# Kernel optimization log

Hardware: AMD Instinct MI355X
Metric: run time of the kernel (lower is better)

Reference implementation:

```python
import jax, jax.numpy as jnp
import numpy as np

EMB = 1024
HEADS = 16
HEAD_DIM = EMB // HEADS
ROPE_BASE = 10000.0


def rotate_half(x):
    # Interleaved rotate: pairs (x0,x1,x2,x3,...) -> (-x1,x0,-x3,x2,...)
    x1 = x[..., ::2]
    x2 = x[..., 1::2]
    return jnp.stack((-x2, x1), axis=-1).reshape(x.shape)


def rope_cos_sin(seq_len, head_dim):
    inv_freq = 1.0 / (ROPE_BASE ** (jnp.arange(0, head_dim, 2, dtype=jnp.float32) / head_dim))
    pos = jnp.arange(seq_len, dtype=jnp.float32)
    freqs = jnp.outer(pos, inv_freq)            # [S, hd/2]
    emb = jnp.concatenate([freqs, freqs], -1)   # [S, hd]  (NOTE: concat, matching source)
    return jnp.cos(emb)[None, None], jnp.sin(emb)[None, None]  # [1,1,S,hd]


def setup_inputs() -> dict:
    key = jax.random.key(0)
    ks = jax.random.split(key, 5)
    B, S = 2, 2048
    x = jax.random.normal(ks[0], (B, S, EMB), dtype=jnp.float32)
    scale = EMB ** -0.5
    Wq = jax.random.normal(ks[1], (EMB, EMB), dtype=jnp.float32) * scale
    Wk = jax.random.normal(ks[2], (EMB, EMB), dtype=jnp.float32) * scale
    Wv = jax.random.normal(ks[3], (EMB, EMB), dtype=jnp.float32) * scale
    Wo = jax.random.normal(ks[4], (EMB, EMB), dtype=jnp.float32) * scale
    return {"x": x, "Wq": Wq, "Wk": Wk, "Wv": Wv, "Wo": Wo}


def reference(x, Wq, Wk, Wv, Wo):
    B, S, E = x.shape
    def shape_heads(t):
        return t.reshape(B, S, HEADS, HEAD_DIM).transpose(0, 2, 1, 3)  # [B,H,S,hd]
    q = shape_heads(x @ Wq.T)
    k = shape_heads(x @ Wk.T)
    v = shape_heads(x @ Wv.T)
    cos, sin = rope_cos_sin(S, HEAD_DIM)
    q = q * cos + rotate_half(q) * sin
    k = k * cos + rotate_half(k) * sin
    scale = HEAD_DIM ** -0.5
    scores = jnp.einsum('bhqd,bhkd->bhqk', q, k) * scale  # [B,H,S,S]
    causal = jnp.triu(jnp.ones((S, S), dtype=bool), k=1)
    scores = jnp.where(causal, -jnp.inf, scores)
    attn = jax.nn.softmax(scores, axis=-1)
    out = jnp.einsum('bhqk,bhkd->bhqd', attn, v)           # [B,H,S,hd]
    out = out.transpose(0, 2, 1, 3).reshape(B, S, E)
    return out @ Wo.T
```

## Files before the change

kernel.cpp:

```cpp
#include <hip/hip_runtime.h>
#include <cstdint>
#include <cstddef>

typedef __bf16 bf16;
typedef __attribute__((ext_vector_type(8))) __bf16 bf16x8;
typedef __attribute__((ext_vector_type(4))) __bf16 bf16x4;
typedef __attribute__((ext_vector_type(4))) float f32x4;

constexpr int kS = 2048;
constexpr int kH = 16;
constexpr int kD = 64;

__device__ __forceinline__ void gload16(const bf16* g, bf16* l) {
  __builtin_amdgcn_global_load_lds((const __attribute__((address_space(1))) void*)g,
                                   (__attribute__((address_space(3))) void*)l, 16, 0, 0);
}

__global__ __launch_bounds__(256) void cast_all_kernel(
    const float* __restrict__ x, const float* __restrict__ wq, const float* __restrict__ wk,
    const float* __restrict__ wv, const float* __restrict__ wo,
    bf16* __restrict__ xb, bf16* __restrict__ wqb, bf16* __restrict__ wkb,
    bf16* __restrict__ wvb, bf16* __restrict__ wob) {
  int idx = blockIdx.x * 256 + threadIdx.x;
  const float* src; bf16* dst; int i;
  if (idx < (1 << 20)) { src = x; dst = xb; i = idx << 2; }
  else {
    int r = idx - (1 << 20);
    int t = r >> 18;
    i = (r & ((1 << 18) - 1)) << 2;
    src = (t == 0) ? wq : (t == 1) ? wk : (t == 2) ? wv : wo;
    dst = (t == 0) ? wqb : (t == 1) ? wkb : (t == 2) ? wvb : wob;
  }
  float4 v = *(const float4*)(src + i);
  bf16x4 o;
  o[0] = (bf16)v.x; o[1] = (bf16)v.y; o[2] = (bf16)v.z; o[3] = (bf16)v.w;
  *(bf16x4*)(dst + i) = o;
}

__global__ __launch_bounds__(256) void gemm_qkv(const bf16* __restrict__ A,
                                                const bf16* __restrict__ wq,
                                                const bf16* __restrict__ wk,
                                                const bf16* __restrict__ wv,
                                                bf16* __restrict__ qo,
                                                bf16* __restrict__ ko,
                                                bf16* __restrict__ vto) {
  __shared__ bf16 As[128 * 32];
  __shared__ bf16 Bs[128 * 32];
  const int tid = threadIdx.x;
  const int w = tid >> 6, l = tid & 63;
  const int wr = w >> 1, wc = w & 1;
  const int lr = l & 15, lg = l >> 4;

  const int fid = (blockIdx.x & 7) * 96 + (blockIdx.x >> 3);
  const int mblk = fid & 31;
  const int ntile = fid >> 5;
  const int which = ntile >> 3;
  const int m0 = mblk * 128;
  const int n0 = (ntile & 7) * 128;
  const bf16* Bw = (which == 0) ? wq : (which == 1) ? wk : wv;

  const int srow = l >> 2;
  const int skcol = (l & 3) << 3;
  const int K = 1024;

  const bf16* aP0 = A + (size_t)(m0 + w * 16 + srow) * K + skcol;
  const bf16* aP1 = A + (size_t)(m0 + 64 + w * 16 + srow) * K + skcol;
  const bf16* bP0 = Bw + (size_t)(n0 + w * 16 + srow) * K + skcol;
  const bf16* bP1 = Bw + (size_t)(n0 + 64 + w * 16 + srow) * K + skcol;
  bf16* aL0 = As + (w * 64 + l) * 8;
  bf16* aL1 = As + ((4 + w) * 64 + l) * 8;
  bf16* bL0 = Bs + (w * 64 + l) * 8;
  bf16* bL1 = Bs + ((4 + w) * 64 + l) * 8;

  f32x4 acc[4][4] = {};

  for (int kt = 0; kt < K; kt += 32) {
    gload16(aP0 + kt, aL0);
    gload16(aP1 + kt, aL1);
    gload16(bP0 + kt, bL0);
    gload16(bP1 + kt, bL1);
    __syncthreads();
    bf16x8 af[4], bfg[4];
#pragma unroll
    for (int mi = 0; mi < 4; mi++)
      af[mi] = *(const bf16x8*)&As[(wr * 64 + mi * 16 + lr) * 32 + lg * 8];
#pragma unroll
    for (int ni = 0; ni < 4; ni++)
      bfg[ni] = *(const bf16x8*)&Bs[(wc * 64 + ni * 16 + lr) * 32 + lg * 8];
#pragma unroll
    for (int mi = 0; mi < 4; mi++)
#pragma unroll
      for (int ni = 0; ni < 4; ni++)
        acc[mi][ni] = __builtin_amdgcn_mfma_f32_16x16x32_bf16(af[mi], bfg[ni], acc[mi][ni], 0, 0, 0);
    __syncthreads();
  }

  float invf_[4];
#pragma unroll
  for (int ni = 0; ni < 4; ni++) {
    int d31 = ((n0 + wc * 64 + ni * 16 + lr) & 63) & 31;
    invf_[ni] = exp2f((float)d31 * -0.41524100480466348f);
  }

#pragma unroll
  for (int mi = 0; mi < 4; mi++) {
#pragma unroll
    for (int ni = 0; ni < 4; ni++) {
#pragma unroll
      for (int r = 0; r < 4; r++) {
        const int m = m0 + wr * 64 + mi * 16 + lg * 4 + r;
        const int n = n0 + wc * 64 + ni * 16 + lr;
        float v = acc[mi][ni][r];
        const int st = m & 2047;
        const size_t bh = (size_t)(m >> 11) * kH + (n >> 6);
        if (which < 2) {
          float vp = __shfl_xor(v, 1);
          const int d = n & 63;
          float th = (float)st * invf_[ni];
          float sth = __sinf(th), cth = __cosf(th);
          float rv = v * cth + ((d & 1) ? vp : -vp) * sth;
          bf16* dst = which ? ko : qo;
          dst[((bh << 11) + st) * kD + (n & 63)] = (bf16)rv;
        } else {
          int pos = (st & ~31) | (((st >> 2) & 3) << 3) | (((st >> 4) & 1) << 2) | (st & 3);
          vto[((bh * kD + (n & 63)) << 11) + pos] = (bf16)v;
        }
      }
    }
  }
}

__global__ __launch_bounds__(256) void gemm_out(const bf16* __restrict__ A,
                                                const bf16* __restrict__ Bw,
                                                float* __restrict__ Cout) {
  __shared__ bf16 As[128 * 32];
  __shared__ bf16 Bs[128 * 32];
  const int tid = threadIdx.x;
  const int w = tid >> 6, l = tid & 63;
  const int wr = w >> 1, wc = w & 1;
  const int lr = l & 15, lg = l >> 4;
  const int m0 = blockIdx.y * 128, n0 = blockIdx.x * 128;
  const int K = 1024, N = 1024;

  const int srow = l >> 2;
  const int skcol = (l & 3) << 3;

  const bf16* aP0 = A + (size_t)(m0 + w * 16 + srow) * K + skcol;
  const bf16* aP1 = A + (size_t)(m0 + 64 + w * 16 + srow) * K + skcol;
  const bf16* bP0 = Bw + (size_t)(n0 + w * 16 + srow) * K + skcol;
  const bf16* bP1 = Bw + (size_t)(n0 + 64 + w * 16 + srow) * K + skcol;
  bf16* aL0 = As + (w * 64 + l) * 8;
  bf16* aL1 = As + ((4 + w) * 64 + l) * 8;
  bf16* bL0 = Bs + (w * 64 + l) * 8;
  bf16* bL1 = Bs + ((4 + w) * 64 + l) * 8;

  f32x4 acc[4][4] = {};

  for (int kt = 0; kt < K; kt += 32) {
    gload16(aP0 + kt, aL0);
    gload16(aP1 + kt, aL1);
    gload16(bP0 + kt, bL0);
    gload16(bP1 + kt, bL1);
    __syncthreads();
    bf16x8 af[4], bfg[4];
#pragma unroll
    for (int mi = 0; mi < 4; mi++)
      af[mi] = *(const bf16x8*)&As[(wr * 64 + mi * 16 + lr) * 32 + lg * 8];
#pragma unroll
    for (int ni = 0; ni < 4; ni++)
      bfg[ni] = *(const bf16x8*)&Bs[(wc * 64 + ni * 16 + lr) * 32 + lg * 8];
#pragma unroll
    for (int mi = 0; mi < 4; mi++)
#pragma unroll
      for (int ni = 0; ni < 4; ni++)
        acc[mi][ni] = __builtin_amdgcn_mfma_f32_16x16x32_bf16(af[mi], bfg[ni], acc[mi][ni], 0, 0, 0);
    __syncthreads();
  }

#pragma unroll
  for (int mi = 0; mi < 4; mi++)
#pragma unroll
    for (int ni = 0; ni < 4; ni++)
#pragma unroll
      for (int r = 0; r < 4; r++) {
        const int m = m0 + wr * 64 + mi * 16 + lg * 4 + r;
        const int n = n0 + wc * 64 + ni * 16 + lr;
        Cout[(size_t)m * N + n] = acc[mi][ni][r];
      }
}


#define STAGE(BUF, KV0)                                                                  \
  {                                                                                      \
    const bf16* kg_ = kh + (size_t)((KV0) + w * 16 + lr) * 64 + lg * 8;                  \
    gload16(kg_,      &Ks[BUF][(w * 2 + 0) * 512 + l * 8]);                              \
    gload16(kg_ + 32, &Ks[BUF][(w * 2 + 1) * 512 + l * 8]);                              \
    const bf16* vg_ = vh + (size_t)(w * 16 + lr) * 2048 + (KV0) + lg * 8;                \
    gload16(vg_,      &Vs[BUF][(w * 2 + 0) * 512 + l * 8]);                              \
    gload16(vg_ + 32, &Vs[BUF][(w * 2 + 1) * 512 + l * 8]);                              \
  }

#define COMPUTE(BUF, DIAG, O, MRUN, LPART, QF, QROW, KVB)                                \
  {                                                                                      \
    bf16x8 kf_[4][2], vf_[4][2];                                                         \
    _Pragma("unroll") for (int s_ = 0; s_ < 4; s_++)                                     \
      _Pragma("unroll") for (int c_ = 0; c_ < 2; c_++)                                   \
        kf_[s_][c_] = *(const bf16x8*)&Ks[BUF][(s_ * 2 + c_) * 512 + l * 8];             \
    _Pragma("unroll") for (int c_ = 0; c_ < 4; c_++)                                     \
      _Pragma("unroll") for (int f_ = 0; f_ < 2; f_++)                                   \
        vf_[c_][f_] = *(const bf16x8*)&Vs[BUF][(c_ * 2 + f_) * 512 + l * 8];             \
    f32x4 sa_[4] = {};                                                                   \
    __builtin_amdgcn_s_setprio(1);                                                       \
    _Pragma("unroll") for (int s_ = 0; s_ < 4; s_++) {                                   \
      sa_[s_] = __builtin_amdgcn_mfma_f32_16x16x32_bf16(kf_[s_][0], QF[0], sa_[s_], 0, 0, 0); \
      sa_[s_] = __builtin_amdgcn_mfma_f32_16x16x32_bf16(kf_[s_][1], QF[1], sa_[s_], 0, 0, 0); \
    }                                                                                    \
    __builtin_amdgcn_s_setprio(0);                                                       \
    float sc_[4][4];                                                                     \
    float tml_ = -1e30f;                                                                 \
    _Pragma("unroll") for (int s_ = 0; s_ < 4; s_++)                                     \
      _Pragma("unroll") for (int r_ = 0; r_ < 4; r_++) {                                 \
        float v_ = sa_[s_][r_] * 0.125f;                                                 \
        if (DIAG) {                                                                      \
          int kk_ = (KVB) + s_ * 16 + lg * 4 + r_;                                       \
          v_ = (kk_ <= (QROW)) ? v_ : -1e30f;                                            \
        }                                                                                \
        sc_[s_][r_] = v_;                                                                \
        tml_ = fmaxf(tml_, v_);                                                          \
      }                                                                                  \
    if (__any(tml_ > MRUN + 20.0f)) {                                                    \
      float tm_ = tml_;                                                                  \
      tm_ = fmaxf(tm_, __shfl_xor(tm_, 16));                                             \
      tm_ = fmaxf(tm_, __shfl_xor(tm_, 32));                                             \
      tm_ = fmaxf(tm_, MRUN);                                                            \
      float f_ = __expf(MRUN - tm_);                                                     \
      _Pragma("unroll") for (int c_ = 0; c_ < 4; c_++) O[c_] *= f_;                      \
      LPART *= f_;                                                                       \
      MRUN = tm_;                                                                        \
    }                                                                                    \
    bf16x8 pf_[2];                                                                       \
    float ts_ = 0.0f;                                                                    \
    _Pragma("unroll") for (int s_ = 0; s_ < 4; s_++)                                     \
      _Pragma("unroll") for (int r_ = 0; r_ < 4; r_++) {                                 \
        float e_ = __expf(sc_[s_][r_] - MRUN);                                           \
        ts_ += e_;                                                                       \
        pf_[s_ >> 1][(s_ & 1) * 4 + r_] = (bf16)e_;                                      \
      }                                                                                  \
    LPART += ts_;                                                                        \
    __builtin_amdgcn_s_setprio(1);                                                       \
    _Pragma("unroll") for (int c_ = 0; c_ < 4; c_++) {                                   \
      O[c_] = __builtin_amdgcn_mfma_f32_16x16x32_bf16(vf_[c_][0], pf_[0], O[c_], 0, 0, 0); \
      O[c_] = __builtin_amdgcn_mfma_f32_16x16x32_bf16(vf_[c_][1], pf_[1], O[c_], 0, 0, 0); \
    }                                                                                    \
    __builtin_amdgcn_s_setprio(0);                                                       \
  }

#define EPILOG(O, LPART, Q0)                                                             \
  {                                                                                      \
    float lt_ = LPART;                                                                   \
    lt_ += __shfl_xor(lt_, 16);                                                          \
    lt_ += __shfl_xor(lt_, 32);                                                          \
    const float inv_ = 1.0f / lt_;                                                       \
    _Pragma("unroll") for (int c_ = 0; c_ < 4; c_++) {                                   \
      bf16x4 ov_;                                                                        \
      _Pragma("unroll") for (int r_ = 0; r_ < 4; r_++) ov_[r_] = (bf16)(O[c_][r_] * inv_); \
      size_t addr_ = ((size_t)(b * kS + (Q0) + lr)) * (kH * kD) + h * 64 + c_ * 16 + lg * 4; \
      *(bf16x4*)&ob[addr_] = ov_;                                                        \
    }                                                                                    \
  }

__global__ __launch_bounds__(256, 2) void attn_kernel(const bf16* __restrict__ qb,
                                                      const bf16* __restrict__ kb,
                                                      const bf16* __restrict__ vtb,
                                                      bf16* __restrict__ ob) {
  __shared__ bf16 Ks[2][4096];
  __shared__ bf16 Vs[2][4096];
  const int tid = threadIdx.x;
  const int w = tid >> 6, l = tid & 63;
  const int lr = l & 15, lg = l >> 4;
  const int bid = blockIdx.x;
  const int bh = bid & 31;
  const int p = bid >> 5;
  const int qtA = 31 - p, qtB = p;
  const bf16* qh = qb + (size_t)bh * (kS * kD);
  const bf16* kh = kb + (size_t)bh * (kS * kD);
  const bf16* vh = vtb + (size_t)bh * (kS * kD);
  const int b = bh >> 4, h = bh & 15;

  STAGE(0, 0)
  __syncthreads();
  int cur = 0;

  {
    const int q0 = qtA * 64 + w * 16;
    const int q = q0 + lr;
    bf16x8 qf[2];
#pragma unroll
    for (int c = 0; c < 2; c++)
      qf[c] = *(const bf16x8*)&qh[(size_t)(q0 + lr) * kD + c * 32 + lg * 8];
    float m_run = 8.0f, lpart = 0.0f;
    f32x4 o[4] = {};
    for (int t = 0; t <= qtA; t++) {
      STAGE(cur ^ 1, (t < qtA) ? (t + 1) * 64 : 0)
      COMPUTE(cur, (t == qtA), o, m_run, lpart, qf, q, t * 64)
      __syncthreads();
      cur ^= 1;
    }
    EPILOG(o, lpart, q0)
  }

  {
    const int q0 = qtB * 64 + w * 16;
    const int q = q0 + lr;
    bf16x8 qf[2];
#pragma unroll
    for (int c = 0; c < 2; c++)
      qf[c] = *(const bf16x8*)&qh[(size_t)(q0 + lr) * kD + c * 32 + lg * 8];
    float m_run = 8.0f, lpart = 0.0f;
    f32x4 o[4] = {};
    for (int t = 0; t <= qtB; t++) {
      if (t < qtB) STAGE(cur ^ 1, (t + 1) * 64)
      COMPUTE(cur, (t == qtB), o, m_run, lpart, qf, q, t * 64)
      __syncthreads();
      cur ^= 1;
    }
    EPILOG(o, lpart, q0)
  }
}

extern "C" void kernel_launch(void* const* d_in, const int* in_sizes, int n_in,
                              void* d_out, int out_size, void* d_ws, size_t ws_size,
                              hipStream_t stream) {
  const float* x  = (const float*)d_in[0];
  const float* wq = (const float*)d_in[1];
  const float* wk = (const float*)d_in[2];
  const float* wv = (const float*)d_in[3];
  const float* wo = (const float*)d_in[4];

  bf16* xb  = (bf16*)d_ws;
  bf16* qb  = xb + (1 << 22);
  bf16* kb  = qb + (1 << 22);
  bf16* vtb = kb + (1 << 22);
  bf16* ab  = vtb + (1 << 22);
  bf16* wqb = ab + (1 << 22);
  bf16* wkb = wqb + (1 << 20);
  bf16* wvb = wkb + (1 << 20);
  bf16* wob = wvb + (1 << 20);

  cast_all_kernel<<<8192, 256, 0, stream>>>(x, wq, wk, wv, wo, xb, wqb, wkb, wvb, wob);
  gemm_qkv<<<768, 256, 0, stream>>>(xb, wqb, wkb, wvb, qb, kb, vtb);
  attn_kernel<<<512, 256, 0, stream>>>(qb, kb, vtb, ab);
  gemm_out<<<dim3(8, 32), 256, 0, stream>>>(ab, wob, (float*)d_out);
}
```

Baseline: 132.8 us.

## Double-buffer LDS tiles with XOR swizzle and MFMA priority in projection GEMMs

Result: faster. 127.9 us (-3.7%).

```diff
diff --git a/kernel.cpp b/kernel.cpp
--- a/kernel.cpp
+++ b/kernel.cpp
@@ -37,6 +37,13 @@
   *(bf16x4*)(dst + i) = o;
 }
 
+
+#define GSTAGE(BUF, KT)                                    \
+  gload16(aP0 + (KT), &As[BUF][(w * 64 + l) * 8]);         \
+  gload16(aP1 + (KT), &As[BUF][((4 + w) * 64 + l) * 8]);   \
+  gload16(bP0 + (KT), &Bs[BUF][(w * 64 + l) * 8]);         \
+  gload16(bP1 + (KT), &Bs[BUF][((4 + w) * 64 + l) * 8]);
+
 __global__ __launch_bounds__(256) void gemm_qkv(const bf16* __restrict__ A,
                                                 const bf16* __restrict__ wq,
                                                 const bf16* __restrict__ wk,
@@ -44,8 +51,8 @@
                                                 bf16* __restrict__ qo,
                                                 bf16* __restrict__ ko,
                                                 bf16* __restrict__ vto) {
-  __shared__ bf16 As[128 * 32];
-  __shared__ bf16 Bs[128 * 32];
+  __shared__ bf16 As[2][128 * 32];
+  __shared__ bf16 Bs[2][128 * 32];
   const int tid = threadIdx.x;
   const int w = tid >> 6, l = tid & 63;
   const int wr = w >> 1, wc = w & 1;
@@ -60,39 +67,38 @@
   const bf16* Bw = (which == 0) ? wq : (which == 1) ? wk : wv;
 
   const int srow = l >> 2;
-  const int skcol = (l & 3) << 3;
+  const int skcol = ((l & 3) ^ ((l >> 3) & 3)) << 3;
   const int K = 1024;
 
   const bf16* aP0 = A + (size_t)(m0 + w * 16 + srow) * K + skcol;
   const bf16* aP1 = A + (size_t)(m0 + 64 + w * 16 + srow) * K + skcol;
   const bf16* bP0 = Bw + (size_t)(n0 + w * 16 + srow) * K + skcol;
   const bf16* bP1 = Bw + (size_t)(n0 + 64 + w * 16 + srow) * K + skcol;
-  bf16* aL0 = As + (w * 64 + l) * 8;
-  bf16* aL1 = As + ((4 + w) * 64 + l) * 8;
-  bf16* bL0 = Bs + (w * 64 + l) * 8;
-  bf16* bL1 = Bs + ((4 + w) * 64 + l) * 8;
 
   f32x4 acc[4][4] = {};
-
+  const int ca = (lg ^ ((lr >> 1) & 3)) * 8;
+
+  GSTAGE(0, 0)
+  __syncthreads();
+  int cur = 0;
   for (int kt = 0; kt < K; kt += 32) {
-    gload16(aP0 + kt, aL0);
-    gload16(aP1 + kt, aL1);
-    gload16(bP0 + kt, bL0);
-    gload16(bP1 + kt, bL1);
-    __syncthreads();
+    if (kt + 32 < K) { GSTAGE(cur ^ 1, kt + 32) }
     bf16x8 af[4], bfg[4];
 #pragma unroll
     for (int mi = 0; mi < 4; mi++)
-      af[mi] = *(const bf16x8*)&As[(wr * 64 + mi * 16 + lr) * 32 + lg * 8];
+      af[mi] = *(const bf16x8*)&As[cur][(wr * 64 + mi * 16 + lr) * 32 + ca];
 #pragma unroll
     for (int ni = 0; ni < 4; ni++)
-      bfg[ni] = *(const bf16x8*)&Bs[(wc * 64 + ni * 16 + lr) * 32 + lg * 8];
+      bfg[ni] = *(const bf16x8*)&Bs[cur][(wc * 64 + ni * 16 + lr) * 32 + ca];
+    __builtin_amdgcn_s_setprio(1);
 #pragma unroll
     for (int mi = 0; mi < 4; mi++)
 #pragma unroll
       for (int ni = 0; ni < 4; ni++)
         acc[mi][ni] = __builtin_amdgcn_mfma_f32_16x16x32_bf16(af[mi], bfg[ni], acc[mi][ni], 0, 0, 0);
+    __builtin_amdgcn_s_setprio(0);
     __syncthreads();
+    cur ^= 1;
   }
 
   float invf_[4];
@@ -133,8 +139,8 @@
 __global__ __launch_bounds__(256) void gemm_out(const bf16* __restrict__ A,
                                                 const bf16* __restrict__ Bw,
                                                 float* __restrict__ Cout) {
-  __shared__ bf16 As[128 * 32];
-  __shared__ bf16 Bs[128 * 32];
+  __shared__ bf16 As[2][128 * 32];
+  __shared__ bf16 Bs[2][128 * 32];
   const int tid = threadIdx.x;
   const int w = tid >> 6, l = tid & 63;
   const int wr = w >> 1, wc = w & 1;
@@ -143,38 +149,37 @@
   const int K = 1024, N = 1024;
 
   const int srow = l >> 2;
-  const int skcol = (l & 3) << 3;
+  const int skcol = ((l & 3) ^ ((l >> 3) & 3)) << 3;
 
   const bf16* aP0 = A + (size_t)(m0 + w * 16 + srow) * K + skcol;
   const bf16* aP1 = A + (size_t)(m0 + 64 + w * 16 + srow) * K + skcol;
   const bf16* bP0 = Bw + (size_t)(n0 + w * 16 + srow) * K + skcol;
   const bf16* bP1 = Bw + (size_t)(n0 + 64 + w * 16 + srow) * K + skcol;
-  bf16* aL0 = As + (w * 64 + l) * 8;
-  bf16* aL1 = As + ((4 + w) * 64 + l) * 8;
-  bf16* bL0 = Bs + (w * 64 + l) * 8;
-  bf16* bL1 = Bs + ((4 + w) * 64 + l) * 8;
 
   f32x4 acc[4][4] = {};
-
+  const int ca = (lg ^ ((lr >> 1) & 3)) * 8;
+
+  GSTAGE(0, 0)
+  __syncthreads();
+  int cur = 0;
   for (int kt = 0; kt < K; kt += 32) {
-    gload16(aP0 + kt, aL0);
-    gload16(aP1 + kt, aL1);
-    gload16(bP0 + kt, bL0);
-    gload16(bP1 + kt, bL1);
-    __syncthreads();
+    if (kt + 32 < K) { GSTAGE(cur ^ 1, kt + 32) }
     bf16x8 af[4], bfg[4];
 #pragma unroll
     for (int mi = 0; mi < 4; mi++)
-      af[mi] = *(const bf16x8*)&As[(wr * 64 + mi * 16 + lr) * 32 + lg * 8];
+      af[mi] = *(const bf16x8*)&As[cur][(wr * 64 + mi * 16 + lr) * 32 + ca];
 #pragma unroll
     for (int ni = 0; ni < 4; ni++)
-      bfg[ni] = *(const bf16x8*)&Bs[(wc * 64 + ni * 16 + lr) * 32 + lg * 8];
+      bfg[ni] = *(const bf16x8*)&Bs[cur][(wc * 64 + ni * 16 + lr) * 32 + ca];
+    __builtin_amdgcn_s_setprio(1);
 #pragma unroll
     for (int mi = 0; mi < 4; mi++)
 #pragma unroll
       for (int ni = 0; ni < 4; ni++)
         acc[mi][ni] = __builtin_amdgcn_mfma_f32_16x16x32_bf16(af[mi], bfg[ni], acc[mi][ni], 0, 0, 0);
+    __builtin_amdgcn_s_setprio(0);
     __syncthreads();
+    cur ^= 1;
   }
 
 #pragma unroll
```
